# Kernel tuning notes

Measured on AMD Instinct MI355X. Metric: run time of the kernel, lower is better.

The kernel has to match this reference:

```python
import jax, jax.numpy as jnp
import numpy as np

B, S, D = 512, 199, 512
SKILL_MAX, PRO_MAX = 300, 20000
TIME_SLOTS = 200


def setup_inputs() -> dict:
    key = jax.random.key(0)
    ks = jax.random.split(key, 24)
    u = lambda k, shape: jax.random.uniform(k, shape, dtype=jnp.float32)
    ri = lambda k, shape, hi: jax.random.randint(k, shape, 0, hi, dtype=jnp.int32)
    d = D
    inp = {
        "last_problem": ri(ks[0], (B, S), PRO_MAX),
        "last_skill": ri(ks[1], (B, S), SKILL_MAX),
        "last_ans": ri(ks[2], (B, S), 2),
        "next_problem": ri(ks[3], (B, S), PRO_MAX),
        "next_skill": ri(ks[4], (B, S), SKILL_MAX),
        "next_ans": ri(ks[5], (B, S), 2),
        # learned parameters (torch.rand init -> uniform[0,1) for embeds/states)
        "skill_embed": u(ks[6], (SKILL_MAX, d)),
        "ans_embed": u(ks[7], (2, d)),
        "time_embed": u(ks[8], (TIME_SLOTS, d)),
        "ls_state": u(ks[9], (1, d)),
        "skill_state0": u(ks[10], (S, d)),
        # Linear weights stored as [in, out] (x @ W + b)
        "W_sf": (u(ks[11], (2 * d, d)) - 0.5) * 0.05, "b_sf": jnp.zeros((d,), jnp.float32),
        "W_af": (u(ks[12], (2 * d, d)) - 0.5) * 0.05, "b_af": jnp.zeros((d,), jnp.float32),
        "W_ss": (u(ks[13], (2 * d, d)) - 0.5) * 0.05, "b_ss": jnp.zeros((d,), jnp.float32),
        "W_as": (u(ks[14], (2 * d, d)) - 0.5) * 0.05, "b_as": jnp.zeros((d,), jnp.float32),
        "W_o1": (u(ks[15], (3 * d, d)) - 0.5) * 0.05, "b_o1": jnp.zeros((d,), jnp.float32),
        "W_o2": (u(ks[16], (d, 1)) - 0.5) * 0.05, "b_o2": jnp.zeros((1,), jnp.float32),
    }
    return inp


def _forward(floats, next_skill, next_ans):
    (skill_embed, ans_embed, time_embed, ls_state, skill_state0,
     W_sf, b_sf, W_af, b_af, W_ss, b_ss, W_as, b_as,
     W_o1, b_o1, W_o2, b_o2) = floats
    batch, seq = next_skill.shape
    d = skill_embed.shape[1]
    skill_max = skill_embed.shape[0]

    next_pro_embed = skill_embed[next_skill]                 # [B,S,d]
    next_X = next_pro_embed + ans_embed[next_ans]            # [B,S,d]
    time1_emb = time_embed[1]                                # all_time_gap == 1 everywhere
    batch_idx = jnp.arange(batch)

    all_state0 = jnp.broadcast_to(ls_state, (batch, d)) + jnp.zeros((batch, d), ls_state.dtype)
    skill_buf0 = jnp.broadcast_to(skill_state0[None], (batch, seq, d)) + jnp.zeros((batch, seq, d), skill_state0.dtype)
    last_time0 = jnp.zeros((batch, skill_max), jnp.int32)

    def step(carry, xs):
        all_state, skill_buf, last_time = carry
        now_step, now_pro, now_X, sk_idx = xs             # scalar, [B,d], [B,d], [B]
        t_last = last_time[batch_idx, sk_idx]             # [B]
        last_sk = skill_buf[batch_idx, t_last]            # [B,d] gather over history slot
        gap_emb = time_embed[now_step - t_last]           # [B,d]
        f_sk = jax.nn.sigmoid(jnp.concatenate([last_sk, gap_emb], -1) @ W_sf + b_sf)
        last_sk = last_sk * f_sk
        f_all = jax.nn.sigmoid(jnp.concatenate([all_state, jnp.broadcast_to(time1_emb, all_state.shape)], -1) @ W_af + b_af)
        last_all = all_state * f_all
        final = jnp.concatenate([last_all, last_sk, now_pro], -1)   # [B,3d]
        h = jax.nn.relu(final @ W_o1 + b_o1)
        P = jax.nn.sigmoid(h @ W_o2 + b_o2)[:, 0]                    # [B]
        new_all = last_all + jnp.tanh(jnp.concatenate([last_all, now_X], -1) @ W_as + b_as)
        new_sk = last_sk + jnp.tanh(jnp.concatenate([last_sk, now_X], -1) @ W_ss + b_ss)
        last_time = last_time.at[batch_idx, sk_idx].set(now_step)
        skill_buf = jax.lax.dynamic_update_slice_in_dim(skill_buf, new_sk[:, None, :], now_step, axis=1)
        return (new_all, skill_buf, last_time), P

    xs = (jnp.arange(seq, dtype=jnp.int32),
          jnp.swapaxes(next_pro_embed, 0, 1),
          jnp.swapaxes(next_X, 0, 1),
          next_skill.T)
    _, P_all = jax.lax.scan(step, (all_state0, skill_buf0, last_time0), xs)
    return P_all.T                                               # [B,S]


def reference(last_problem, last_skill, last_ans, next_problem, next_skill, next_ans,
              skill_embed, ans_embed, time_embed, ls_state, skill_state0,
              W_sf, b_sf, W_af, b_af, W_ss, b_ss, W_as, b_as, W_o1, b_o1, W_o2, b_o2):
    floats = (skill_embed, ans_embed, time_embed, ls_state, skill_state0,
              W_sf, b_sf, W_af, b_af, W_ss, b_ss, W_as, b_as, W_o1, b_o1, W_o2, b_o2)
    return _forward(floats, next_skill, next_ans)
```

## Files before the change

### kernel.cpp

```cpp
#include <hip/hip_runtime.h>

typedef unsigned short ushort_t;
typedef unsigned int uint_t;
typedef unsigned long long ull_t;
typedef __attribute__((ext_vector_type(8))) short short8;
typedef __attribute__((ext_vector_type(4))) float f32x4;
typedef __attribute__((ext_vector_type(4))) uint_t uint4v;

constexpr size_t OFF_WSFT  = 0;
constexpr size_t OFF_WAFT  = OFF_WSFT  + 512*512*2;
constexpr size_t OFF_WO1AT = OFF_WAFT  + 512*512*2;
constexpr size_t OFF_WO1BT = OFF_WO1AT + 512*512*2;
constexpr size_t OFF_WAST  = OFF_WO1BT + 512*512*2;
constexpr size_t OFF_WSST  = OFF_WAST  + 512*512*2;
constexpr size_t OFF_GAPS  = OFF_WSST  + 512*512*2;
constexpr size_t OFF_CAFV  = OFF_GAPS  + 200*512*4;
constexpr size_t OFF_XA    = OFF_CAFV  + 512*4;
constexpr size_t OFF_XS    = OFF_XA    + 600*512*4;
constexpr size_t OFF_PROJ  = OFF_XS    + 600*512*4;
constexpr size_t OFF_LAG   = OFF_PROJ  + 300*512*4;
constexpr size_t OFF_LSG   = OFF_LAG   + 512*512*2;
constexpr size_t OFF_ASG   = OFF_LSG   + 512*512*2;
constexpr size_t OFF_ISKR  = OFF_ASG   + 512*512*2;
constexpr size_t OFF_IGAP  = OFF_ISKR  + 199*512*4;
constexpr size_t OFF_IXR   = OFF_IGAP  + 199*512*4;
constexpr size_t OFF_ISK   = OFF_IXR   + 199*512*4;
constexpr size_t OFF_BAR   = OFF_ISK   + 199*512*4;
constexpr size_t OFF_SKB   = OFF_BAR   + 16*64*4;
constexpr size_t WS_NEED   = OFF_SKB   + (size_t)512*199*512*2;

__device__ __forceinline__ ushort_t f2bf(float f) {
  union { float f; uint_t u; } v; v.f = f;
  uint_t u = v.u;
  return (ushort_t)((u + 0x7FFFu + ((u >> 16) & 1u)) >> 16);
}
__device__ __forceinline__ float bf2f(ushort_t h) {
  union { uint_t u; float f; } v; v.u = ((uint_t)h) << 16;
  return v.f;
}
__device__ __forceinline__ void coh_st4(void* p, uint_t v) {
  __hip_atomic_store((uint_t*)p, v, __ATOMIC_RELAXED, __HIP_MEMORY_SCOPE_AGENT);
}

__global__ void rekt_prep(const float* __restrict__ ls_state, const float* __restrict__ skill_state0,
                          const float* __restrict__ W_sf, const float* __restrict__ W_af,
                          const float* __restrict__ W_ss, const float* __restrict__ W_as,
                          const float* __restrict__ W_o1,
                          float* __restrict__ d_out, char* __restrict__ ws) {
  ushort_t* WSFT  = (ushort_t*)(ws + OFF_WSFT);
  ushort_t* WAFT  = (ushort_t*)(ws + OFF_WAFT);
  ushort_t* WO1AT = (ushort_t*)(ws + OFF_WO1AT);
  ushort_t* WO1BT = (ushort_t*)(ws + OFF_WO1BT);
  ushort_t* WAST  = (ushort_t*)(ws + OFF_WAST);
  ushort_t* WSST  = (ushort_t*)(ws + OFF_WSST);
  ushort_t* ASG   = (ushort_t*)(ws + OFF_ASG);
  int*      BARp  = (int*)(ws + OFF_BAR);
  ushort_t* SKB   = (ushort_t*)(ws + OFF_SKB);

  const size_t t0 = (size_t)blockIdx.x * blockDim.x + threadIdx.x;
  const size_t st = (size_t)gridDim.x * blockDim.x;

  for (size_t i = t0; i < 512*512; i += st) {
    const int k = (int)(i >> 9), n = (int)(i & 511);
    const size_t d = (size_t)n * 512 + k;
    WSFT[d]  = f2bf(W_sf[i]);
    WAFT[d]  = f2bf(W_af[i]);
    WAST[d]  = f2bf(W_as[i]);
    WSST[d]  = f2bf(W_ss[i]);
    WO1AT[d] = f2bf(W_o1[i]);
    WO1BT[d] = f2bf(W_o1[i + (size_t)512*512]);
  }
  for (size_t i = t0; i < 512*512; i += st) ASG[i] = f2bf(ls_state[i & 511]);
  for (size_t i = t0; i < 512*512; i += st) {
    const size_t b = i >> 9, n = i & 511;
    SKB[(b * 199) * 512 + n] = f2bf(skill_state0[n]);
  }
  for (size_t i = t0; i < 512*199; i += st) d_out[i] = 0.f;
  for (size_t i = t0; i < 16*64; i += st) BARp[i] = 0;
}

__global__ void rekt_tab(const float* __restrict__ se, const float* __restrict__ ae,
                         const float* __restrict__ te,
                         const float* __restrict__ W_sf, const float* __restrict__ b_sf,
                         const float* __restrict__ W_af, const float* __restrict__ b_af,
                         const float* __restrict__ W_ss, const float* __restrict__ b_ss,
                         const float* __restrict__ W_as, const float* __restrict__ b_as,
                         const float* __restrict__ W_o1, const float* __restrict__ b_o1,
                         char* __restrict__ ws) {
  __shared__ float ar[512];
  const int n = threadIdx.x;
  const int bid = blockIdx.x;
  const float* W; const float* bias; float* dst;
  if (bid < 600) {
    const int a = bid / 300, sk = bid % 300;
    ar[n] = se[(size_t)sk*512 + n] + ae[(size_t)a*512 + n];
    W = W_as + (size_t)512*512; bias = b_as; dst = (float*)(ws + OFF_XA) + (size_t)bid*512;
  } else if (bid < 1200) {
    const int r = bid - 600, a = r / 300, sk = r % 300;
    ar[n] = se[(size_t)sk*512 + n] + ae[(size_t)a*512 + n];
    W = W_ss + (size_t)512*512; bias = b_ss; dst = (float*)(ws + OFF_XS) + (size_t)r*512;
  } else if (bid < 1500) {
    const int r = bid - 1200;
    ar[n] = se[(size_t)r*512 + n];
    W = W_o1 + (size_t)1024*512; bias = b_o1; dst = (float*)(ws + OFF_PROJ) + (size_t)r*512;
  } else if (bid < 1700) {
    const int t = bid - 1500;
    ar[n] = te[(size_t)t*512 + n];
    W = W_sf + (size_t)512*512; bias = b_sf; dst = (float*)(ws + OFF_GAPS) + (size_t)t*512;
  } else {
    ar[n] = te[512 + n];
    W = W_af + (size_t)512*512; bias = b_af; dst = (float*)(ws + OFF_CAFV);
  }
  __syncthreads();
  float acc = bias[n];
  for (int k = 0; k < 512; ++k) acc = fmaf(ar[k], W[(size_t)k*512 + n], acc);
  dst[n] = acc;
}

__global__ void rekt_idx(const int* __restrict__ next_skill, const int* __restrict__ next_ans,
                         char* __restrict__ ws) {
  int* ISKR = (int*)(ws + OFF_ISKR);
  int* IGAP = (int*)(ws + OFF_IGAP);
  int* IXR  = (int*)(ws + OFF_IXR);
  int* ISK  = (int*)(ws + OFF_ISK);
  __shared__ int lt[300];
  const int b = blockIdx.x;
  for (int i = threadIdx.x; i < 300; i += blockDim.x) lt[i] = 0;
  __syncthreads();
  if (threadIdx.x == 0) {
    for (int s = 0; s < 199; ++s) {
      const int sk = next_skill[b * 199 + s];
      const int tl = lt[sk];
      ISKR[s * 512 + b] = b * 199 + tl;
      IGAP[s * 512 + b] = s - tl;
      IXR [s * 512 + b] = next_ans[b * 199 + s] * 300 + sk;
      ISK [s * 512 + b] = sk;
      lt[sk] = s;
    }
  }
}

__device__ __forceinline__ void bar_sig(int* flg, int sl, int val) {
  __syncthreads();
  if (threadIdx.x == 0)
    __hip_atomic_store(flg + sl, val, __ATOMIC_RELAXED, __HIP_MEMORY_SCOPE_AGENT);
}
__device__ __forceinline__ void bar_wait(const int* flg, int val) {
  if (threadIdx.x < 16) {
    int guard = 0;
    while (__hip_atomic_load(flg + threadIdx.x, __ATOMIC_RELAXED, __HIP_MEMORY_SCOPE_AGENT) < val) {
      __builtin_amdgcn_s_sleep(1);
      if (++guard > (1 << 22)) break;
    }
  }
  __syncthreads();
}

template<bool GATHER>
__device__ __forceinline__ void stage2(short* Ta, short* Tb,
                                       const ushort_t* __restrict__ baseA, const int* rowsA,
                                       const ushort_t* __restrict__ baseB, int tid) {
  uint4v va[4], vb[4];
  int dst[4];
#pragma unroll
  for (int t = 0; t < 4; ++t) {
    const int i = t * 512 + tid;
    const int r = i >> 6, gi = i & 63;
    const size_t rowA = GATHER ? (size_t)rowsA[r] : (size_t)r;
    const ushort_t* pa = baseA + rowA * 512 + gi * 8;
    const ushort_t* pb = baseB + (size_t)r * 512 + gi * 8;
    asm volatile("global_load_dwordx4 %0, %1, off sc0 sc1" : "=v"(va[t]) : "v"(pa));
    asm volatile("global_load_dwordx4 %0, %1, off sc0 sc1" : "=v"(vb[t]) : "v"(pb));
    dst[t] = r * 512 + ((gi ^ (r & 7)) << 3);
  }
  asm volatile("s_waitcnt vmcnt(0)" ::: "memory");
  __builtin_amdgcn_sched_barrier(0);
#pragma unroll
  for (int t = 0; t < 4; ++t) {
    *reinterpret_cast<uint4v*>(Ta + dst[t]) = va[t];
    *reinterpret_cast<uint4v*>(Tb + dst[t]) = vb[t];
  }
}

#define MFMA(a, b, c) __builtin_amdgcn_mfma_f32_16x16x32_bf16((a), (b), (c), 0, 0, 0)

__global__ __launch_bounds__(512, 1) void rekt_main(
    const float* __restrict__ w_o2,
    float* __restrict__ d_out, char* __restrict__ ws) {

  const ushort_t* WSFT  = (const ushort_t*)(ws + OFF_WSFT);
  const ushort_t* WAFT  = (const ushort_t*)(ws + OFF_WAFT);
  const ushort_t* WO1AT = (const ushort_t*)(ws + OFF_WO1AT);
  const ushort_t* WO1BT = (const ushort_t*)(ws + OFF_WO1BT);
  const ushort_t* WAST  = (const ushort_t*)(ws + OFF_WAST);
  const ushort_t* WSST  = (const ushort_t*)(ws + OFF_WSST);
  const float* GAPS = (const float*)(ws + OFF_GAPS);
  const float* CAFV = (const float*)(ws + OFF_CAFV);
  const float* XA   = (const float*)(ws + OFF_XA);
  const float* XS   = (const float*)(ws + OFF_XS);
  const float* PROJ = (const float*)(ws + OFF_PROJ);
  ushort_t* LAG = (ushort_t*)(ws + OFF_LAG);
  ushort_t* LSG = (ushort_t*)(ws + OFF_LSG);
  ushort_t* ASG = (ushort_t*)(ws + OFF_ASG);
  const int* ISKR = (const int*)(ws + OFF_ISKR);
  const int* IGAP = (const int*)(ws + OFF_IGAP);
  const int* IXR  = (const int*)(ws + OFF_IXR);
  const int* ISK  = (const int*)(ws + OFF_ISK);
  int*      FLG = (int*)(ws + OFF_BAR);
  ushort_t* SKB = (ushort_t*)(ws + OFF_SKB);

  __shared__ __align__(16) short Ta[32 * 512];
  __shared__ __align__(16) short Tb[32 * 512];
  __shared__ float Hbuf[32 * 144];
  __shared__ int sk_s[32], gap_s[32], xr_s[32], skrow_s[32];

  const int tid = threadIdx.x;
  const int lane = tid & 63, w = tid >> 6;
  const int cc = lane & 15, hi = lane >> 4;
  const int m = w & 1, nt = (w >> 1) & 1, setB = w >> 2;
  const int g = blockIdx.x >> 4, sl = blockIdx.x & 15;
  const int b0 = g << 5;
  const int nc = sl * 32 + nt * 16 + cc;
  const int ncl = nt * 16 + cc;
  const int arow = m * 16 + cc;
  const int r0 = m * 16 + hi * 4;
  const int aswz = (cc & 7) << 3;
  int* flgA = FLG + g * 64;
  int* flgB = FLG + g * 64 + 32;

  const float cafv = CAFV[nc];
  const float wo2v = w_o2[nc];

  const ushort_t* BA = (setB ? WAFT  : WSFT ) + (size_t)nc * 512 + hi * 8;
  const ushort_t* BH = (setB ? WO1BT : WO1AT) + (size_t)nc * 512 + hi * 8;
  const ushort_t* BU = (setB ? WSST  : WAST ) + (size_t)nc * 512 + hi * 8;

  for (int s = 0; s < 199; ++s) {
    if (tid < 32) {
      const int o = s * 512 + b0 + tid;
      sk_s[tid]    = ISK[o];
      gap_s[tid]   = IGAP[o];
      xr_s[tid]    = IXR[o];
      skrow_s[tid] = ISKR[o];
    }
    short8 Bf[16];
#pragma unroll
    for (int j = 0; j < 16; ++j) Bf[j] = *reinterpret_cast<const short8*>(BA + j * 32);

    bar_wait(flgB, s);

    stage2<true>(Ta, Tb, SKB, skrow_s, ASG + (size_t)b0 * 512, tid);
    __syncthreads();

    f32x4 accA = {0.f, 0.f, 0.f, 0.f};
    {
      const short* a0 = (setB ? Tb : Ta) + arow * 512;
#pragma unroll
      for (int j = 0; j < 16; ++j) {
        const short8 a = *reinterpret_cast<const short8*>(a0 + (((j * 4 + hi) << 3) ^ aswz));
        accA = MFMA(a, Bf[j], accA);
      }
    }

    if (setB == 0) {
#pragma unroll
      for (int q = 0; q < 4; ++q) {
        const int r = r0 + q;
        const float F = accA[q] + GAPS[(size_t)gap_s[r] * 512 + nc];
        const float sg = 1.f / (1.f + __expf(-F));
        const float skg = bf2f((ushort_t)Ta[r * 512 + (((nc >> 3) ^ (r & 7)) << 3) + (nc & 7)]);
        const uint_t pz = f2bf(skg * sg);
        const uint_t oz = (uint_t)__shfl_xor((int)pz, 1, 64);
        if (!(cc & 1)) coh_st4(LSG + (size_t)(b0 + r) * 512 + nc, pz | (oz << 16));
      }
    } else {
#pragma unroll
      for (int q = 0; q < 4; ++q) {
        const int r = r0 + q;
        const float G = accA[q] + cafv;
        const float sg = 1.f / (1.f + __expf(-G));
        const float asv = bf2f((ushort_t)Tb[r * 512 + (((nc >> 3) ^ (r & 7)) << 3) + (nc & 7)]);
        const uint_t pz = f2bf(asv * sg);
        const uint_t oz = (uint_t)__shfl_xor((int)pz, 1, 64);
        if (!(cc & 1)) coh_st4(LAG + (size_t)(b0 + r) * 512 + nc, pz | (oz << 16));
      }
    }
    bar_sig(flgA, sl, s + 1);

    short8 B1[16], B2[16];
#pragma unroll
    for (int j = 0; j < 16; ++j) {
      B1[j] = *reinterpret_cast<const short8*>(BH + j * 32);
      B2[j] = *reinterpret_cast<const short8*>(BU + j * 32);
    }
    bar_wait(flgA, s + 1);

    stage2<false>(Ta, Tb, LAG + (size_t)b0 * 512, nullptr, LSG + (size_t)b0 * 512, tid);
    __syncthreads();

    f32x4 acc1 = {0.f, 0.f, 0.f, 0.f}, acc2 = {0.f, 0.f, 0.f, 0.f};
    {
      const short* a0 = (setB ? Tb : Ta) + arow * 512;
#pragma unroll
      for (int j = 0; j < 16; ++j) {
        const short8 a = *reinterpret_cast<const short8*>(a0 + (((j * 4 + hi) << 3) ^ aswz));
        acc1 = MFMA(a, B1[j], acc1);
        acc2 = MFMA(a, B2[j], acc2);
      }
    }

    if (setB == 0) {
#pragma unroll
      for (int q = 0; q < 4; ++q) Hbuf[(r0 + q) * 144 + ncl] = acc1[q];
    }
    __syncthreads();

    float pv[4];
    if (setB == 0) {
#pragma unroll
      for (int q = 0; q < 4; ++q) {
        const int r = r0 + q;
        float x = acc2[q] + XA[(size_t)xr_s[r] * 512 + nc];
        x = fminf(fmaxf(x, -12.f), 12.f);
        const float e = __expf(2.f * x);
        const float lav = bf2f((ushort_t)Ta[r * 512 + (((nc >> 3) ^ (r & 7)) << 3) + (nc & 7)]);
        const uint_t pz = f2bf(lav + (e - 1.f) / (e + 1.f));
        const uint_t oz = (uint_t)__shfl_xor((int)pz, 1, 64);
        if (!(cc & 1)) coh_st4(ASG + (size_t)(b0 + r) * 512 + nc, pz | (oz << 16));
      }
    } else {
#pragma unroll
      for (int q = 0; q < 4; ++q) {
        const int r = r0 + q;
        const float h = fmaxf(Hbuf[r * 144 + ncl] + acc1[q] + PROJ[(size_t)sk_s[r] * 512 + nc], 0.f);
        pv[q] = h * wo2v;

        float y = acc2[q] + XS[(size_t)xr_s[r] * 512 + nc];
        y = fminf(fmaxf(y, -12.f), 12.f);
        const float e = __expf(2.f * y);
        const float lsv = bf2f((ushort_t)Tb[r * 512 + (((nc >> 3) ^ (r & 7)) << 3) + (nc & 7)]);
        const uint_t pz = f2bf(lsv + (e - 1.f) / (e + 1.f));
        const uint_t oz = (uint_t)__shfl_xor((int)pz, 1, 64);
        if (!(cc & 1)) coh_st4(SKB + ((size_t)(b0 + r) * 199 + s) * 512 + nc, pz | (oz << 16));
      }
    }
    bar_sig(flgB, sl, s + 1);

    if (setB == 1) {
#pragma unroll
      for (int msk = 1; msk < 16; msk <<= 1) {
#pragma unroll
        for (int q = 0; q < 4; ++q) pv[q] += __shfl_xor(pv[q], msk, 64);
      }
      if (cc == 0) {
#pragma unroll
        for (int q = 0; q < 4; ++q) atomicAdd(&d_out[(size_t)(b0 + r0 + q) * 199 + s], pv[q]);
      }
    }
  }
}

__global__ void rekt_out(float* __restrict__ d_out, const float* __restrict__ b_o2) {
  const int i = blockIdx.x * blockDim.x + threadIdx.x;
  if (i < 512 * 199) {
    const float v = d_out[i] + b_o2[0];
    d_out[i] = 1.f / (1.f + __expf(-v));
  }
}

extern "C" void kernel_launch(void* const* d_in, const int* in_sizes, int n_in,
                              void* d_out, int out_size, void* d_ws, size_t ws_size,
                              hipStream_t stream) {
  const int*   next_skill   = (const int*)d_in[4];
  const int*   next_ans     = (const int*)d_in[5];
  const float* skill_embed  = (const float*)d_in[6];
  const float* ans_embed    = (const float*)d_in[7];
  const float* time_embed   = (const float*)d_in[8];
  const float* ls_state     = (const float*)d_in[9];
  const float* skill_state0 = (const float*)d_in[10];
  const float* W_sf = (const float*)d_in[11];
  const float* b_sf = (const float*)d_in[12];
  const float* W_af = (const float*)d_in[13];
  const float* b_af = (const float*)d_in[14];
  const float* W_ss = (const float*)d_in[15];
  const float* b_ss = (const float*)d_in[16];
  const float* W_as = (const float*)d_in[17];
  const float* b_as = (const float*)d_in[18];
  const float* W_o1 = (const float*)d_in[19];
  const float* b_o1 = (const float*)d_in[20];
  const float* W_o2 = (const float*)d_in[21];
  const float* b_o2 = (const float*)d_in[22];
  float* out = (float*)d_out;
  char*  ws  = (char*)d_ws;

  if (ws_size < WS_NEED) return;

  rekt_prep<<<dim3(2048), dim3(256), 0, stream>>>(
      ls_state, skill_state0, W_sf, W_af, W_ss, W_as, W_o1, out, ws);
  rekt_tab<<<dim3(1701), dim3(512), 0, stream>>>(
      skill_embed, ans_embed, time_embed,
      W_sf, b_sf, W_af, b_af, W_ss, b_ss, W_as, b_as, W_o1, b_o1, ws);
  rekt_idx<<<dim3(512), dim3(64), 0, stream>>>(next_skill, next_ans, ws);

  rekt_main<<<dim3(256), dim3(512), 0, stream>>>(W_o2, out, ws);

  rekt_out<<<dim3((512 * 199 + 255) / 256), dim3(256), 0, stream>>>(out, b_o2);
}
```

Before: 4.441 ms.

## Decouple skill-state recurrence into dependency-depth rounds, leaving only all-state serial

Each row's dependency depth along its skill chain is computed in advance, and rows are bucketed into per-depth lists. The skill-state update and its W_o1 projection contribution then run as batched GEMMs over all rows of a depth level, one kernel launch per round. The remaining sequential kernel carries only the all-state recurrence, with fewer cross-block barriers per step. Depths beyond the cap are merged into the last round, which could break ordering if a skill chain is that deep. It also adds a large workspace for the stored projections and twelve extra launches.

```diff
diff --git a/kernel.cpp b/kernel.cpp
--- a/kernel.cpp
+++ b/kernel.cpp
@@ -2,7 +2,6 @@
 
 typedef unsigned short ushort_t;
 typedef unsigned int uint_t;
-typedef unsigned long long ull_t;
 typedef __attribute__((ext_vector_type(8))) short short8;
 typedef __attribute__((ext_vector_type(4))) float f32x4;
 typedef __attribute__((ext_vector_type(4))) uint_t uint4v;
@@ -18,16 +17,21 @@
 constexpr size_t OFF_XA    = OFF_CAFV  + 512*4;
 constexpr size_t OFF_XS    = OFF_XA    + 600*512*4;
 constexpr size_t OFF_PROJ  = OFF_XS    + 600*512*4;
-constexpr size_t OFF_LAG   = OFF_PROJ  + 300*512*4;
-constexpr size_t OFF_LSG   = OFF_LAG   + 512*512*2;
-constexpr size_t OFF_ASG   = OFF_LSG   + 512*512*2;
+constexpr size_t OFF_ASG   = OFF_PROJ  + 300*512*4;
 constexpr size_t OFF_ISKR  = OFF_ASG   + 512*512*2;
 constexpr size_t OFF_IGAP  = OFF_ISKR  + 199*512*4;
 constexpr size_t OFF_IXR   = OFF_IGAP  + 199*512*4;
 constexpr size_t OFF_ISK   = OFF_IXR   + 199*512*4;
-constexpr size_t OFF_BAR   = OFF_ISK   + 199*512*4;
-constexpr size_t OFF_SKB   = OFF_BAR   + 16*64*4;
-constexpr size_t WS_NEED   = OFF_SKB   + (size_t)512*199*512*2;
+constexpr size_t OFF_DEP   = OFF_ISK   + 199*512*4;
+constexpr size_t OFF_LCNT  = OFF_DEP   + 199*512*4;
+constexpr size_t OFF_LROW  = OFF_LCNT  + 16*4;
+constexpr size_t OFF_FLG   = OFF_LROW  + (size_t)12*101888*4;
+constexpr size_t OFF_HS    = OFF_FLG   + 16*8*4;
+constexpr size_t OFF_SKB   = OFF_HS    + (size_t)101888*512*2;
+constexpr size_t WS_NEED   = OFF_SKB   + (size_t)101888*512*2;
+
+constexpr int NROWS = 199 * 512;
+constexpr int ROUNDS = 12;
 
 __device__ __forceinline__ ushort_t f2bf(float f) {
   union { float f; uint_t u; } v; v.f = f;
@@ -41,6 +45,8 @@
 __device__ __forceinline__ void coh_st4(void* p, uint_t v) {
   __hip_atomic_store((uint_t*)p, v, __ATOMIC_RELAXED, __HIP_MEMORY_SCOPE_AGENT);
 }
+
+#define MFMA(a, b, c) __builtin_amdgcn_mfma_f32_16x16x32_bf16((a), (b), (c), 0, 0, 0)
 
 __global__ void rekt_prep(const float* __restrict__ ls_state, const float* __restrict__ skill_state0,
                           const float* __restrict__ W_sf, const float* __restrict__ W_af,
@@ -54,7 +60,8 @@
   ushort_t* WAST  = (ushort_t*)(ws + OFF_WAST);
   ushort_t* WSST  = (ushort_t*)(ws + OFF_WSST);
   ushort_t* ASG   = (ushort_t*)(ws + OFF_ASG);
-  int*      BARp  = (int*)(ws + OFF_BAR);
+  int*      LCNT  = (int*)(ws + OFF_LCNT);
+  int*      FLG   = (int*)(ws + OFF_FLG);
   ushort_t* SKB   = (ushort_t*)(ws + OFF_SKB);
 
   const size_t t0 = (size_t)blockIdx.x * blockDim.x + threadIdx.x;
@@ -75,8 +82,9 @@
     const size_t b = i >> 9, n = i & 511;
     SKB[(b * 199) * 512 + n] = f2bf(skill_state0[n]);
   }
-  for (size_t i = t0; i < 512*199; i += st) d_out[i] = 0.f;
-  for (size_t i = t0; i < 16*64; i += st) BARp[i] = 0;
+  for (size_t i = t0; i < (size_t)512*199; i += st) d_out[i] = 0.f;
+  for (size_t i = t0; i < 16; i += st) LCNT[i] = 0;
+  for (size_t i = t0; i < 16*8; i += st) FLG[i] = 0;
 }
 
 __global__ void rekt_tab(const float* __restrict__ se, const float* __restrict__ ae,
@@ -123,7 +131,9 @@
   int* IGAP = (int*)(ws + OFF_IGAP);
   int* IXR  = (int*)(ws + OFF_IXR);
   int* ISK  = (int*)(ws + OFF_ISK);
+  int* DEP  = (int*)(ws + OFF_DEP);
   __shared__ int lt[300];
+  __shared__ int pd[199];
   const int b = blockIdx.x;
   for (int i = threadIdx.x; i < 300; i += blockDim.x) lt[i] = 0;
   __syncthreads();
@@ -135,227 +145,288 @@
       IGAP[s * 512 + b] = s - tl;
       IXR [s * 512 + b] = next_ans[b * 199 + s] * 300 + sk;
       ISK [s * 512 + b] = sk;
+      const int d = (s == 0) ? 0 : (pd[tl] + 1);
+      pd[s] = d;
+      DEP[s * 512 + b] = d;
       lt[sk] = s;
     }
   }
 }
 
-__device__ __forceinline__ void bar_sig(int* flg, int sl, int val) {
-  __syncthreads();
-  if (threadIdx.x == 0)
-    __hip_atomic_store(flg + sl, val, __ATOMIC_RELAXED, __HIP_MEMORY_SCOPE_AGENT);
-}
-__device__ __forceinline__ void bar_wait(const int* flg, int val) {
-  if (threadIdx.x < 16) {
-    int guard = 0;
-    while (__hip_atomic_load(flg + threadIdx.x, __ATOMIC_RELAXED, __HIP_MEMORY_SCOPE_AGENT) < val) {
-      __builtin_amdgcn_s_sleep(1);
-      if (++guard > (1 << 22)) break;
-    }
-  }
-  __syncthreads();
-}
-
-template<bool GATHER>
-__device__ __forceinline__ void stage2(short* Ta, short* Tb,
-                                       const ushort_t* __restrict__ baseA, const int* rowsA,
-                                       const ushort_t* __restrict__ baseB, int tid) {
-  uint4v va[4], vb[4];
-  int dst[4];
-#pragma unroll
-  for (int t = 0; t < 4; ++t) {
-    const int i = t * 512 + tid;
-    const int r = i >> 6, gi = i & 63;
-    const size_t rowA = GATHER ? (size_t)rowsA[r] : (size_t)r;
-    const ushort_t* pa = baseA + rowA * 512 + gi * 8;
-    const ushort_t* pb = baseB + (size_t)r * 512 + gi * 8;
-    asm volatile("global_load_dwordx4 %0, %1, off sc0 sc1" : "=v"(va[t]) : "v"(pa));
-    asm volatile("global_load_dwordx4 %0, %1, off sc0 sc1" : "=v"(vb[t]) : "v"(pb));
-    dst[t] = r * 512 + ((gi ^ (r & 7)) << 3);
-  }
-  asm volatile("s_waitcnt vmcnt(0)" ::: "memory");
-  __builtin_amdgcn_sched_barrier(0);
-#pragma unroll
-  for (int t = 0; t < 4; ++t) {
-    *reinterpret_cast<uint4v*>(Ta + dst[t]) = va[t];
-    *reinterpret_cast<uint4v*>(Tb + dst[t]) = vb[t];
-  }
-}
-
-#define MFMA(a, b, c) __builtin_amdgcn_mfma_f32_16x16x32_bf16((a), (b), (c), 0, 0, 0)
-
-__global__ __launch_bounds__(512, 1) void rekt_main(
-    const float* __restrict__ w_o2,
-    float* __restrict__ d_out, char* __restrict__ ws) {
-
+__global__ void rekt_lists(char* __restrict__ ws) {
+  const int* DEP = (const int*)(ws + OFF_DEP);
+  int* LCNT = (int*)(ws + OFF_LCNT);
+  uint_t* LROW = (uint_t*)(ws + OFF_LROW);
+  const int i = blockIdx.x * blockDim.x + threadIdx.x;
+  if (i < NROWS) {
+    const int s = i >> 9, b = i & 511;
+    int d = DEP[i];
+    if (d > ROUNDS - 1) d = ROUNDS - 1;
+    const int pos = atomicAdd(&LCNT[d], 1);
+    LROW[(size_t)d * NROWS + pos] = ((uint_t)s << 16) | (uint_t)b;
+  }
+}
+
+__global__ __launch_bounds__(512, 1) void rekt_skill(int round, char* __restrict__ ws) {
   const ushort_t* WSFT  = (const ushort_t*)(ws + OFF_WSFT);
-  const ushort_t* WAFT  = (const ushort_t*)(ws + OFF_WAFT);
-  const ushort_t* WO1AT = (const ushort_t*)(ws + OFF_WO1AT);
+  const ushort_t* WSST  = (const ushort_t*)(ws + OFF_WSST);
   const ushort_t* WO1BT = (const ushort_t*)(ws + OFF_WO1BT);
-  const ushort_t* WAST  = (const ushort_t*)(ws + OFF_WAST);
-  const ushort_t* WSST  = (const ushort_t*)(ws + OFF_WSST);
   const float* GAPS = (const float*)(ws + OFF_GAPS);
-  const float* CAFV = (const float*)(ws + OFF_CAFV);
-  const float* XA   = (const float*)(ws + OFF_XA);
   const float* XS   = (const float*)(ws + OFF_XS);
-  const float* PROJ = (const float*)(ws + OFF_PROJ);
-  ushort_t* LAG = (ushort_t*)(ws + OFF_LAG);
-  ushort_t* LSG = (ushort_t*)(ws + OFF_LSG);
-  ushort_t* ASG = (ushort_t*)(ws + OFF_ASG);
   const int* ISKR = (const int*)(ws + OFF_ISKR);
   const int* IGAP = (const int*)(ws + OFF_IGAP);
   const int* IXR  = (const int*)(ws + OFF_IXR);
-  const int* ISK  = (const int*)(ws + OFF_ISK);
-  int*      FLG = (int*)(ws + OFF_BAR);
+  const int* LCNT = (const int*)(ws + OFF_LCNT);
+  const uint_t* LROW = (const uint_t*)(ws + OFF_LROW) + (size_t)round * NROWS;
+  ushort_t* HS  = (ushort_t*)(ws + OFF_HS);
   ushort_t* SKB = (ushort_t*)(ws + OFF_SKB);
 
   __shared__ __align__(16) short Ta[32 * 512];
-  __shared__ __align__(16) short Tb[32 * 512];
-  __shared__ float Hbuf[32 * 144];
-  __shared__ int sk_s[32], gap_s[32], xr_s[32], skrow_s[32];
-
+  __shared__ __align__(16) short LSb[32 * 512];
+  __shared__ int gap_s[32], xr_s[32], skrow_s[32], dst_s[32];
+
+  const int nrows = LCNT[round];
+  const int ntiles = (nrows + 31) >> 5;
   const int tid = threadIdx.x;
   const int lane = tid & 63, w = tid >> 6;
   const int cc = lane & 15, hi = lane >> 4;
-  const int m = w & 1, nt = (w >> 1) & 1, setB = w >> 2;
-  const int g = blockIdx.x >> 4, sl = blockIdx.x & 15;
+  const int aswz = (cc & 7) << 3;
+
+  for (int tile = blockIdx.x; tile < ntiles; tile += gridDim.x) {
+    if (tid < 32) {
+      int idx = tile * 32 + tid;
+      if (idx >= nrows) idx = nrows - 1;
+      const uint_t rid = LROW[idx];
+      const int s = (int)(rid >> 16), b = (int)(rid & 0xffff);
+      const int o = s * 512 + b;
+      gap_s[tid] = IGAP[o];
+      xr_s[tid]  = IXR[o];
+      skrow_s[tid] = ISKR[o];
+      dst_s[tid] = b * 199 + s;
+    }
+    __syncthreads();
+
+#pragma unroll
+    for (int t = 0; t < 4; ++t) {
+      const int i = t * 512 + tid;
+      const int r = i >> 6, gi = i & 63;
+      const uint4v v = *reinterpret_cast<const uint4v*>(SKB + (size_t)skrow_s[r] * 512 + gi * 8);
+      *reinterpret_cast<uint4v*>(Ta + r * 512 + ((gi ^ (r & 7)) << 3)) = v;
+    }
+    __syncthreads();
+
+#pragma unroll
+    for (int t = 0; t < 4; ++t) {
+      const int colb = w * 64 + t * 16;
+      const int col = colb + cc;
+      const ushort_t* bp = WSFT + (size_t)col * 512 + hi * 8;
+      f32x4 a0 = {0.f,0.f,0.f,0.f}, a1 = {0.f,0.f,0.f,0.f};
+#pragma unroll
+      for (int j = 0; j < 16; ++j) {
+        const short8 b8 = *reinterpret_cast<const short8*>(bp + j * 32);
+        const int go = ((j * 4 + hi) << 3) ^ aswz;
+        a0 = MFMA(*reinterpret_cast<const short8*>(Ta + cc * 512 + go), b8, a0);
+        a1 = MFMA(*reinterpret_cast<const short8*>(Ta + (16 + cc) * 512 + go), b8, a1);
+      }
+#pragma unroll
+      for (int m = 0; m < 2; ++m) {
+        const f32x4 acc = m ? a1 : a0;
+#pragma unroll
+        for (int q = 0; q < 4; ++q) {
+          const int r = m * 16 + hi * 4 + q;
+          const int si = r * 512 + ((((col >> 3) ^ (r & 7)) << 3) | (col & 7));
+          const float F = acc[q] + GAPS[(size_t)gap_s[r] * 512 + col];
+          const float ls = bf2f((ushort_t)Ta[si]) * (1.f / (1.f + __expf(-F)));
+          const uint_t pz = f2bf(ls);
+          const uint_t oz = (uint_t)__shfl_xor((int)pz, 1, 64);
+          if (!(cc & 1)) *reinterpret_cast<uint_t*>(LSb + si) = pz | (oz << 16);
+        }
+      }
+    }
+    __syncthreads();
+
+#pragma unroll
+    for (int t = 0; t < 4; ++t) {
+      const int colb = w * 64 + t * 16;
+      const int col = colb + cc;
+      const ushort_t* bp2 = WSST  + (size_t)col * 512 + hi * 8;
+      const ushort_t* bp3 = WO1BT + (size_t)col * 512 + hi * 8;
+      f32x4 n0 = {0.f,0.f,0.f,0.f}, n1 = n0, h0 = n0, h1 = n0;
+#pragma unroll
+      for (int j = 0; j < 16; ++j) {
+        const int go = ((j * 4 + hi) << 3) ^ aswz;
+        const short8 a0 = *reinterpret_cast<const short8*>(LSb + cc * 512 + go);
+        const short8 a1 = *reinterpret_cast<const short8*>(LSb + (16 + cc) * 512 + go);
+        const short8 b2 = *reinterpret_cast<const short8*>(bp2 + j * 32);
+        const short8 b3 = *reinterpret_cast<const short8*>(bp3 + j * 32);
+        n0 = MFMA(a0, b2, n0); n1 = MFMA(a1, b2, n1);
+        h0 = MFMA(a0, b3, h0); h1 = MFMA(a1, b3, h1);
+      }
+#pragma unroll
+      for (int m = 0; m < 2; ++m) {
+        const f32x4 nn = m ? n1 : n0;
+        const f32x4 hh = m ? h1 : h0;
+#pragma unroll
+        for (int q = 0; q < 4; ++q) {
+          const int r = m * 16 + hi * 4 + q;
+          const int si = r * 512 + ((((col >> 3) ^ (r & 7)) << 3) | (col & 7));
+          float y = nn[q] + XS[(size_t)xr_s[r] * 512 + col];
+          y = fminf(fmaxf(y, -12.f), 12.f);
+          const float e = __expf(2.f * y);
+          const float skv = bf2f((ushort_t)LSb[si]) + (e - 1.f) / (e + 1.f);
+          const uint_t pz = f2bf(skv);
+          const uint_t oz = (uint_t)__shfl_xor((int)pz, 1, 64);
+          const uint_t hz = f2bf(hh[q]);
+          const uint_t ho = (uint_t)__shfl_xor((int)hz, 1, 64);
+          if (!(cc & 1)) {
+            *reinterpret_cast<uint_t*>(SKB + (size_t)dst_s[r] * 512 + col) = pz | (oz << 16);
+            *reinterpret_cast<uint_t*>(HS  + (size_t)dst_s[r] * 512 + col) = hz | (ho << 16);
+          }
+        }
+      }
+    }
+    __syncthreads();
+  }
+}
+
+__global__ __launch_bounds__(512, 1) void rekt_all(
+    const float* __restrict__ w_o2,
+    float* __restrict__ d_out, char* __restrict__ ws) {
+
+  const ushort_t* WAFT  = (const ushort_t*)(ws + OFF_WAFT);
+  const ushort_t* WO1AT = (const ushort_t*)(ws + OFF_WO1AT);
+  const ushort_t* WAST  = (const ushort_t*)(ws + OFF_WAST);
+  const float* CAFV = (const float*)(ws + OFF_CAFV);
+  const float* XA   = (const float*)(ws + OFF_XA);
+  const float* PROJ = (const float*)(ws + OFF_PROJ);
+  ushort_t* ASG = (ushort_t*)(ws + OFF_ASG);
+  const int* IXR = (const int*)(ws + OFF_IXR);
+  const int* ISK = (const int*)(ws + OFF_ISK);
+  int* FLG = (int*)(ws + OFF_FLG);
+  const ushort_t* HS = (const ushort_t*)(ws + OFF_HS);
+
+  __shared__ __align__(16) short Tb[32 * 512];
+  __shared__ __align__(16) short LAb[32 * 512];
+  __shared__ int xr_s[32], sk_s[32];
+
+  const int tid = threadIdx.x;
+  const int lane = tid & 63, w = tid >> 6;
+  const int cc = lane & 15, hi = lane >> 4;
+  const int g = blockIdx.x >> 3, sl = blockIdx.x & 7;
   const int b0 = g << 5;
-  const int nc = sl * 32 + nt * 16 + cc;
-  const int ncl = nt * 16 + cc;
-  const int arow = m * 16 + cc;
-  const int r0 = m * 16 + hi * 4;
   const int aswz = (cc & 7) << 3;
-  int* flgA = FLG + g * 64;
-  int* flgB = FLG + g * 64 + 32;
-
-  const float cafv = CAFV[nc];
-  const float wo2v = w_o2[nc];
-
-  const ushort_t* BA = (setB ? WAFT  : WSFT ) + (size_t)nc * 512 + hi * 8;
-  const ushort_t* BH = (setB ? WO1BT : WO1AT) + (size_t)nc * 512 + hi * 8;
-  const ushort_t* BU = (setB ? WSST  : WAST ) + (size_t)nc * 512 + hi * 8;
+  int* flg = FLG + g * 8;
+
+  const int mB = w & 1, ntB = w >> 1;
+  const int colB = sl * 64 + ntB * 16 + cc;
+  const float wo2v = w_o2[colB];
 
   for (int s = 0; s < 199; ++s) {
     if (tid < 32) {
       const int o = s * 512 + b0 + tid;
-      sk_s[tid]    = ISK[o];
-      gap_s[tid]   = IGAP[o];
-      xr_s[tid]    = IXR[o];
-      skrow_s[tid] = ISKR[o];
-    }
-    short8 Bf[16];
-#pragma unroll
-    for (int j = 0; j < 16; ++j) Bf[j] = *reinterpret_cast<const short8*>(BA + j * 32);
-
-    bar_wait(flgB, s);
-
-    stage2<true>(Ta, Tb, SKB, skrow_s, ASG + (size_t)b0 * 512, tid);
-    __syncthreads();
-
-    f32x4 accA = {0.f, 0.f, 0.f, 0.f};
+      xr_s[tid] = IXR[o];
+      sk_s[tid] = ISK[o];
+    }
+    if (tid < 8) {
+      int guard = 0;
+      while (__hip_atomic_load(flg + tid, __ATOMIC_RELAXED, __HIP_MEMORY_SCOPE_AGENT) < s) {
+        __builtin_amdgcn_s_sleep(1);
+        if (++guard > (1 << 22)) break;
+      }
+    }
+    __syncthreads();
+
     {
-      const short* a0 = (setB ? Tb : Ta) + arow * 512;
+      uint4v v[4]; int dst[4];
+#pragma unroll
+      for (int t = 0; t < 4; ++t) {
+        const int i = t * 512 + tid;
+        const int r = i >> 6, gi = i & 63;
+        const ushort_t* p = ASG + (size_t)(b0 + r) * 512 + gi * 8;
+        asm volatile("global_load_dwordx4 %0, %1, off sc0 sc1" : "=v"(v[t]) : "v"(p));
+        dst[t] = r * 512 + ((gi ^ (r & 7)) << 3);
+      }
+      asm volatile("s_waitcnt vmcnt(0)" ::: "memory");
+      __builtin_amdgcn_sched_barrier(0);
+#pragma unroll
+      for (int t = 0; t < 4; ++t) *reinterpret_cast<uint4v*>(Tb + dst[t]) = v[t];
+    }
+    __syncthreads();
+
+#pragma unroll
+    for (int t = 0; t < 4; ++t) {
+      const int col = w * 64 + t * 16 + cc;
+      const ushort_t* bp = WAFT + (size_t)col * 512 + hi * 8;
+      f32x4 a0 = {0.f,0.f,0.f,0.f}, a1 = {0.f,0.f,0.f,0.f};
 #pragma unroll
       for (int j = 0; j < 16; ++j) {
-        const short8 a = *reinterpret_cast<const short8*>(a0 + (((j * 4 + hi) << 3) ^ aswz));
-        accA = MFMA(a, Bf[j], accA);
-      }
-    }
-
-    if (setB == 0) {
-#pragma unroll
-      for (int q = 0; q < 4; ++q) {
-        const int r = r0 + q;
-        const float F = accA[q] + GAPS[(size_t)gap_s[r] * 512 + nc];
-        const float sg = 1.f / (1.f + __expf(-F));
-        const float skg = bf2f((ushort_t)Ta[r * 512 + (((nc >> 3) ^ (r & 7)) << 3) + (nc & 7)]);
-        const uint_t pz = f2bf(skg * sg);
-        const uint_t oz = (uint_t)__shfl_xor((int)pz, 1, 64);
-        if (!(cc & 1)) coh_st4(LSG + (size_t)(b0 + r) * 512 + nc, pz | (oz << 16));
-      }
-    } else {
-#pragma unroll
-      for (int q = 0; q < 4; ++q) {
-        const int r = r0 + q;
-        const float G = accA[q] + cafv;
-        const float sg = 1.f / (1.f + __expf(-G));
-        const float asv = bf2f((ushort_t)Tb[r * 512 + (((nc >> 3) ^ (r & 7)) << 3) + (nc & 7)]);
-        const uint_t pz = f2bf(asv * sg);
-        const uint_t oz = (uint_t)__shfl_xor((int)pz, 1, 64);
-        if (!(cc & 1)) coh_st4(LAG + (size_t)(b0 + r) * 512 + nc, pz | (oz << 16));
-      }
-    }
-    bar_sig(flgA, sl, s + 1);
-
-    short8 B1[16], B2[16];
-#pragma unroll
-    for (int j = 0; j < 16; ++j) {
-      B1[j] = *reinterpret_cast<const short8*>(BH + j * 32);
-      B2[j] = *reinterpret_cast<const short8*>(BU + j * 32);
-    }
-    bar_wait(flgA, s + 1);
-
-    stage2<false>(Ta, Tb, LAG + (size_t)b0 * 512, nullptr, LSG + (size_t)b0 * 512, tid);
-    __syncthreads();
-
-    f32x4 acc1 = {0.f, 0.f, 0.f, 0.f}, acc2 = {0.f, 0.f, 0.f, 0.f};
+        const short8 b8 = *reinterpret_cast<const short8*>(bp + j * 32);
+        const int go = ((j * 4 + hi) << 3) ^ aswz;
+        a0 = MFMA(*reinterpret_cast<const short8*>(Tb + cc * 512 + go), b8, a0);
+        a1 = MFMA(*reinterpret_cast<const short8*>(Tb + (16 + cc) * 512 + go), b8, a1);
+      }
+      const float caf = CAFV[col];
+#pragma unroll
+      for (int m = 0; m < 2; ++m) {
+        const f32x4 acc = m ? a1 : a0;
+#pragma unroll
+        for (int q = 0; q < 4; ++q) {
+          const int r = m * 16 + hi * 4 + q;
+          const int si = r * 512 + ((((col >> 3) ^ (r & 7)) << 3) | (col & 7));
+          const float G = acc[q] + caf;
+          const float la = bf2f((ushort_t)Tb[si]) * (1.f / (1.f + __expf(-G)));
+          const uint_t pz = f2bf(la);
+          const uint_t oz = (uint_t)__shfl_xor((int)pz, 1, 64);
+          if (!(cc & 1)) *reinterpret_cast<uint_t*>(LAb + si) = pz | (oz << 16);
+        }
+      }
+    }
+    __syncthreads();
+
+    f32x4 accN = {0.f,0.f,0.f,0.f}, accH = {0.f,0.f,0.f,0.f};
     {
-      const short* a0 = (setB ? Tb : Ta) + arow * 512;
+      const ushort_t* bpN = WAST  + (size_t)colB * 512 + hi * 8;
+      const ushort_t* bpH = WO1AT + (size_t)colB * 512 + hi * 8;
 #pragma unroll
       for (int j = 0; j < 16; ++j) {
-        const short8 a = *reinterpret_cast<const short8*>(a0 + (((j * 4 + hi) << 3) ^ aswz));
-        acc1 = MFMA(a, B1[j], acc1);
-        acc2 = MFMA(a, B2[j], acc2);
-      }
-    }
-
-    if (setB == 0) {
-#pragma unroll
-      for (int q = 0; q < 4; ++q) Hbuf[(r0 + q) * 144 + ncl] = acc1[q];
-    }
-    __syncthreads();
-
+        const int go = ((j * 4 + hi) << 3) ^ aswz;
+        const short8 a = *reinterpret_cast<const short8*>(LAb + (mB * 16 + cc) * 512 + go);
+        accN = MFMA(a, *reinterpret_cast<const short8*>(bpN + j * 32), accN);
+        accH = MFMA(a, *reinterpret_cast<const short8*>(bpH + j * 32), accH);
+      }
+    }
     float pv[4];
-    if (setB == 0) {
-#pragma unroll
-      for (int q = 0; q < 4; ++q) {
-        const int r = r0 + q;
-        float x = acc2[q] + XA[(size_t)xr_s[r] * 512 + nc];
-        x = fminf(fmaxf(x, -12.f), 12.f);
-        const float e = __expf(2.f * x);
-        const float lav = bf2f((ushort_t)Ta[r * 512 + (((nc >> 3) ^ (r & 7)) << 3) + (nc & 7)]);
-        const uint_t pz = f2bf(lav + (e - 1.f) / (e + 1.f));
-        const uint_t oz = (uint_t)__shfl_xor((int)pz, 1, 64);
-        if (!(cc & 1)) coh_st4(ASG + (size_t)(b0 + r) * 512 + nc, pz | (oz << 16));
-      }
-    } else {
-#pragma unroll
-      for (int q = 0; q < 4; ++q) {
-        const int r = r0 + q;
-        const float h = fmaxf(Hbuf[r * 144 + ncl] + acc1[q] + PROJ[(size_t)sk_s[r] * 512 + nc], 0.f);
-        pv[q] = h * wo2v;
-
-        float y = acc2[q] + XS[(size_t)xr_s[r] * 512 + nc];
-        y = fminf(fmaxf(y, -12.f), 12.f);
-        const float e = __expf(2.f * y);
-        const float lsv = bf2f((ushort_t)Tb[r * 512 + (((nc >> 3) ^ (r & 7)) << 3) + (nc & 7)]);
-        const uint_t pz = f2bf(lsv + (e - 1.f) / (e + 1.f));
-        const uint_t oz = (uint_t)__shfl_xor((int)pz, 1, 64);
-        if (!(cc & 1)) coh_st4(SKB + ((size_t)(b0 + r) * 199 + s) * 512 + nc, pz | (oz << 16));
-      }
-    }
-    bar_sig(flgB, sl, s + 1);
-
-    if (setB == 1) {
-#pragma unroll
-      for (int msk = 1; msk < 16; msk <<= 1) {
-#pragma unroll
-        for (int q = 0; q < 4; ++q) pv[q] += __shfl_xor(pv[q], msk, 64);
-      }
-      if (cc == 0) {
-#pragma unroll
-        for (int q = 0; q < 4; ++q) atomicAdd(&d_out[(size_t)(b0 + r0 + q) * 199 + s], pv[q]);
-      }
+#pragma unroll
+    for (int q = 0; q < 4; ++q) {
+      const int r = mB * 16 + hi * 4 + q;
+      const int si = r * 512 + ((((colB >> 3) ^ (r & 7)) << 3) | (colB & 7));
+      const float lav = bf2f((ushort_t)LAb[si]);
+      float x = accN[q] + XA[(size_t)xr_s[r] * 512 + colB];
+      x = fminf(fmaxf(x, -12.f), 12.f);
+      const float e = __expf(2.f * x);
+      const float asv = lav + (e - 1.f) / (e + 1.f);
+      const uint_t pz = f2bf(asv);
+      const uint_t oz = (uint_t)__shfl_xor((int)pz, 1, 64);
+      if (!(cc & 1)) coh_st4(ASG + (size_t)(b0 + r) * 512 + colB, pz | (oz << 16));
+
+      const float hsv = bf2f(HS[((size_t)(b0 + r) * 199 + s) * 512 + colB]);
+      const float h = fmaxf(accH[q] + hsv + PROJ[(size_t)sk_s[r] * 512 + colB], 0.f);
+      pv[q] = h * wo2v;
+    }
+
+    __syncthreads();
+    if (tid == 0)
+      __hip_atomic_store(flg + sl, s + 1, __ATOMIC_RELAXED, __HIP_MEMORY_SCOPE_AGENT);
+
+#pragma unroll
+    for (int msk = 1; msk < 16; msk <<= 1) {
+#pragma unroll
+      for (int q = 0; q < 4; ++q) pv[q] += __shfl_xor(pv[q], msk, 64);
+    }
+    if (cc == 0) {
+#pragma unroll
+      for (int q = 0; q < 4; ++q)
+        atomicAdd(&d_out[(size_t)(b0 + mB * 16 + hi * 4 + q) * 199 + s], pv[q]);
     }
   }
 }
@@ -401,8 +472,12 @@
       skill_embed, ans_embed, time_embed,
       W_sf, b_sf, W_af, b_af, W_ss, b_ss, W_as, b_as, W_o1, b_o1, ws);
   rekt_idx<<<dim3(512), dim3(64), 0, stream>>>(next_skill, next_ans, ws);
-
-  rekt_main<<<dim3(256), dim3(512), 0, stream>>>(W_o2, out, ws);
+  rekt_lists<<<dim3((NROWS + 255) / 256), dim3(256), 0, stream>>>(ws);
+
+  for (int k = 0; k < ROUNDS; ++k)
+    rekt_skill<<<dim3(2048), dim3(512), 0, stream>>>(k, ws);
+
+  rekt_all<<<dim3(128), dim3(512), 0, stream>>>(W_o2, out, ws);
 
   rekt_out<<<dim3((512 * 199 + 255) / 256), dim3(256), 0, stream>>>(out, b_o2);
 }
```

Result: slower. 8.747 ms (+97.0%).
